# Performance work log

Measured on AMD Instinct MI355X. Metric: run time of the kernel, lower is better.

Reference implementation:

```python
import jax, jax.numpy as jnp
import numpy as np

B, C, H, W = 8, 128, 64, 64
C8, C2 = C // 8, C // 2


def conv1x1(x, w, b):
    # x: [B,Cin,H,W], w: [Cout,Cin], b: [Cout]
    return jnp.einsum('bchw,oc->bohw', x, w) + b[None, :, None, None]


def maxpool2(x):
    # 2x2 stride-2 max pool on [B,C,H,W]
    b, c, h, w = x.shape
    return x.reshape(b, c, h // 2, 2, w // 2, 2).max(axis=(3, 5))


def setup_inputs() -> dict:
    key = jax.random.key(0)
    ks = jax.random.split(key, 10)
    s_in = 1.0 / np.sqrt(C)
    s_c2 = 1.0 / np.sqrt(C2)
    return {
        'x': jax.random.normal(ks[0], (B, C, H, W), dtype=jnp.float32),
        'w_theta': jax.random.uniform(ks[1], (C8, C), jnp.float32, -s_in, s_in),
        'b_theta': jax.random.uniform(ks[2], (C8,), jnp.float32, -s_in, s_in),
        'w_phi': jax.random.uniform(ks[3], (C8, C), jnp.float32, -s_in, s_in),
        'b_phi': jax.random.uniform(ks[4], (C8,), jnp.float32, -s_in, s_in),
        'w_g': jax.random.uniform(ks[5], (C2, C), jnp.float32, -s_in, s_in),
        'b_g': jax.random.uniform(ks[6], (C2,), jnp.float32, -s_in, s_in),
        'w_attn': jax.random.uniform(ks[7], (C, C2), jnp.float32, -s_c2, s_c2),
        'b_attn': jax.random.uniform(ks[8], (C,), jnp.float32, -s_c2, s_c2),
        'sigma': jnp.zeros((1,), dtype=jnp.float32),
    }


def reference(x, w_theta, b_theta, w_phi, b_phi, w_g, b_g, w_attn, b_attn, sigma):
    b, ch, h, w = x.shape
    n, m = h * w, (h * w) // 4
    theta = conv1x1(x, w_theta, b_theta).reshape(b, ch // 8, n)          # [B,C8,N]
    phi = maxpool2(conv1x1(x, w_phi, b_phi)).reshape(b, ch // 8, m)      # [B,C8,M]
    attn = jax.nn.softmax(jnp.einsum('bdn,bdm->bnm', theta, phi), axis=-1)  # [B,N,M]
    g = maxpool2(conv1x1(x, w_g, b_g)).reshape(b, ch // 2, m)            # [B,C2,M]
    attn_g = jnp.einsum('bcm,bnm->bcn', g, attn).reshape(b, ch // 2, h, w)
    attn_g = conv1x1(attn_g, w_attn, b_attn)
    return x + sigma[0] * attn_g
```

## Files before the change

kernel.cpp:

```cpp
#include <hip/hip_runtime.h>
#include <hip/hip_bf16.h>
#include <math.h>
#include <string.h>

#define Bn 8
#define Cn 128
#define Nn 4096
#define Mn 1024
#define C8n 16
#define C2n 64

typedef __attribute__((ext_vector_type(8))) short short8;
typedef __attribute__((ext_vector_type(4))) float floatx4;
typedef __attribute__((ext_vector_type(4))) unsigned short ushortx4;

typedef const __attribute__((address_space(1))) void gv_t;
typedef __attribute__((address_space(3))) void lv_t;

__device__ __forceinline__ unsigned short f2bf(float f) {
    union { float f; unsigned u; } v; v.f = f;
    unsigned r = v.u + 0x7fff + ((v.u >> 16) & 1);
    return (unsigned short)(r >> 16);
}
__device__ __forceinline__ unsigned pk2(float a, float b) {
    __hip_bfloat162 h = __float22bfloat162_rn(make_float2(a, b));
    union { __hip_bfloat162 h2; unsigned u; } cv;
    cv.h2 = h;
    return cv.u;
}

__global__ __launch_bounds__(256) void k1_pre(
    const float* __restrict__ x,
    const float* __restrict__ w_theta, const float* __restrict__ b_theta,
    const float* __restrict__ w_phi,   const float* __restrict__ b_phi,
    const float* __restrict__ w_g,     const float* __restrict__ b_g,
    unsigned short* __restrict__ thA,
    unsigned short* __restrict__ phB,
    unsigned short* __restrict__ gB)
{
    __shared__ unsigned short wA[6 * 4 * 64 * 8];
    __shared__ unsigned short xB[8 * 4 * 64 * 8];
    __shared__ unsigned short pool[80][33];
    __shared__ float biases[96];

    const int t    = threadIdx.x;
    const int b    = blockIdx.x & 7;
    const int h2   = blockIdx.x >> 3;
    const int wv   = t >> 6;
    const int lane = t & 63;
    const int q    = lane >> 4;
    const int l15  = lane & 15;
    const float L2E = 1.4426950408889634f;

    if (t < 96)
        biases[t] = (t < 16) ? b_theta[t] * L2E
                  : (t < 32) ? b_phi[t - 16] : b_g[t - 32];

    #pragma unroll
    for (int k = 0; k < 12; ++k) {
        int u  = t + k * 256;
        int oc = u >> 5, c4 = u & 31;
        const float* src = (oc < 16) ? (w_theta + oc * Cn)
                         : (oc < 32) ? (w_phi + (oc - 16) * Cn)
                                     : (w_g + (oc - 32) * Cn);
        float4 wv4 = *(const float4*)(src + c4 * 4);
        float sc = (oc < 16) ? L2E : 1.f;
        int c = c4 * 4;
        int ot = oc >> 4, kc = c >> 5, qq = (c >> 3) & 3, jj = c & 7;
        uint2 pk = { pk2(wv4.x * sc, wv4.y * sc), pk2(wv4.z * sc, wv4.w * sc) };
        *(uint2*)(wA + (((ot * 4 + kc) * 64 + qq * 16 + (oc & 15)) * 8 + jj)) = pk;
    }

    const float* xb = x + (size_t)b * Cn * Nn + h2 * 128;
    #pragma unroll
    for (int k = 0; k < 16; ++k) {
        int u   = t + k * 256;
        int pos = u & 127, c4 = u >> 7;
        int c   = c4 * 4;
        float v0 = xb[(size_t)(c + 0) * Nn + pos];
        float v1 = xb[(size_t)(c + 1) * Nn + pos];
        float v2 = xb[(size_t)(c + 2) * Nn + pos];
        float v3 = xb[(size_t)(c + 3) * Nn + pos];
        int pt = pos >> 4, kc = c >> 5, qq = (c >> 3) & 3, jj = c & 7;
        uint2 pk = { pk2(v0, v1), pk2(v2, v3) };
        *(uint2*)(xB + (((pt * 4 + kc) * 64 + qq * 16 + (pos & 15)) * 8 + jj)) = pk;
    }
    __syncthreads();

    floatx4 acc[6][2];
    #pragma unroll
    for (int ot = 0; ot < 6; ++ot)
        #pragma unroll
        for (int p2 = 0; p2 < 2; ++p2) acc[ot][p2] = (floatx4){0.f, 0.f, 0.f, 0.f};

    #pragma unroll
    for (int kc = 0; kc < 4; ++kc) {
        short8 Bf0 = *(const short8*)(xB + ((wv * 4 + kc) * 64 + lane) * 8);
        short8 Bf1 = *(const short8*)(xB + (((wv + 4) * 4 + kc) * 64 + lane) * 8);
        #pragma unroll
        for (int ot = 0; ot < 6; ++ot) {
            short8 Af = *(const short8*)(wA + ((ot * 4 + kc) * 64 + lane) * 8);
            acc[ot][0] = __builtin_amdgcn_mfma_f32_16x16x32_bf16(Af, Bf0, acc[ot][0], 0, 0, 0);
            acc[ot][1] = __builtin_amdgcn_mfma_f32_16x16x32_bf16(Af, Bf1, acc[ot][1], 0, 0, 0);
        }
    }

    #pragma unroll
    for (int p2 = 0; p2 < 2; ++p2) {
        const int pt = wv + p2 * 4;
        float v0 = acc[0][p2][0] + biases[q * 4 + 0];
        float v1 = acc[0][p2][1] + biases[q * 4 + 1];
        float v2 = acc[0][p2][2] + biases[q * 4 + 2];
        float v3 = acc[0][p2][3] + biases[q * 4 + 3];
        uint2 pk = { pk2(v0, v1), pk2(v2, v3) };
        *(uint2*)(thA + ((((size_t)b * 256 + h2 * 8 + pt) * 2 + (q >> 1)) * 128
                         + l15 * 8 + (q & 1) * 4)) = pk;
    }

    #pragma unroll
    for (int ot = 1; ot < 6; ++ot) {
        #pragma unroll
        for (int r = 0; r < 4; ++r) {
            float vmax = fmaxf(acc[ot][0][r], acc[ot][1][r]);
            float pmax = fmaxf(vmax, __shfl_xor(vmax, 1, 64));
            if ((l15 & 1) == 0) {
                int oc = (ot - 1) * 16 + q * 4 + r;
                int w2 = wv * 8 + (l15 >> 1);
                pool[oc][w2] = f2bf(pmax + biases[16 + oc]);
            }
        }
    }
    __syncthreads();

    if (t < 64) {
        int w2h = t >> 5, ml = (t >> 1) & 15, dh = t & 1;
        int w2 = w2h * 16 + ml;
        ushortx4 lo, hi;
        #pragma unroll
        for (int j = 0; j < 4; ++j) { lo[j] = pool[dh * 8 + j][w2];
                                      hi[j] = pool[dh * 8 + 4 + j][w2]; }
        unsigned short* dst = phB + (((size_t)b * 64 + h2 * 2 + w2h) * 2 + dh) * 128 + ml * 8;
        *(ushortx4*)dst = lo;
        *(ushortx4*)(dst + 4) = hi;
    }
    {
        int c = t >> 2, sq = t & 3;
        ushortx4 lo, hi;
        #pragma unroll
        for (int j = 0; j < 8; ++j) {
            int w2 = (j & 1) * 16 + sq * 4 + (j >> 1);
            unsigned short v = pool[16 + c][w2];
            if (j < 4) lo[j] = v; else hi[j - 4] = v;
        }
        unsigned short* dst = gB + ((((size_t)b * 32 + h2) * 4 + (c >> 4)) * 4 + sq) * 128
                              + (c & 15) * 8;
        *(ushortx4*)dst = lo;
        *(ushortx4*)(dst + 4) = hi;
    }
}

__global__ __launch_bounds__(256, 4) void k2_attn(
    const float* __restrict__ x,
    const unsigned short* __restrict__ thA,
    const unsigned short* __restrict__ phB,
    const unsigned short* __restrict__ gB,
    const float* __restrict__ w_attn, const float* __restrict__ b_attn,
    const float* __restrict__ sigma_p,
    float* __restrict__ out)
{
    __shared__ __attribute__((aligned(16))) char smem[26112];
    char*  Pall  = smem + 20480;
    float* battn = (float*)(smem + 25600);

    const int tid  = threadIdx.x;
    const int wave = tid >> 6;
    const int lane = tid & 63;
    const int q    = lane >> 4;
    const int l15  = lane & 15;
    const int b    = blockIdx.x & 7;
    const int nb   = blockIdx.x >> 3;
    const int t    = wave & 1;
    const int h    = wave >> 1;
    const int ntile = nb * 2 + t;
    const int nw   = ntile * 16;
    char* Pbase = Pall + wave * 1280;

    const float sg = sigma_p[0];

    short8 thf = {};
    if (q < 2)
        thf = *(const short8*)(thA + ((((size_t)b * 256 + ntile) * 2 + q) * 16 + l15) * 8);

    floatx4 O[4];
    #pragma unroll
    for (int cs = 0; cs < 4; ++cs) O[cs] = (floatx4){0.f, 0.f, 0.f, 0.f};
    float L[4] = {0.f, 0.f, 0.f, 0.f};

    const char* phb = (const char*)(phB + (size_t)b * 16384);
    const char* gbb = (const char*)(gB  + (size_t)b * 65536);
    const char* sph = phb + h * 16384;
    const char* sgb = gbb + h * 65536;
    char* mybuf = smem + h * 10240;

    {
        const char* srcp = sph;
        const char* srcg = sgb;
        char* dst = mybuf;
        for (int j = t; j < 5; j += 2) {
            const char* src = (j == 0) ? srcp : (srcg + (j - 1) * 1024);
            __builtin_amdgcn_global_load_lds((gv_t*)(src + lane * 16),
                                             (lv_t*)(dst + j * 1024), 16, 0, 0);
        }
    }

    for (int s = 0; s < 16; ++s) {
        __syncthreads();
        if (s < 15) {
            char* dst = mybuf + ((s + 1) & 1) * 5120;
            const char* srcp = sph + (s + 1) * 1024;
            const char* srcg = sgb + (size_t)(s + 1) * 4096;
            for (int j = t; j < 5; j += 2) {
                const char* src = (j == 0) ? srcp : (srcg + (j - 1) * 1024);
                __builtin_amdgcn_global_load_lds((gv_t*)(src + lane * 16),
                                                 (lv_t*)(dst + j * 1024), 16, 0, 0);
            }
        }
        const char* cbuf = mybuf + (s & 1) * 5120;
        const unsigned short* phis = (const unsigned short*)cbuf;
        const unsigned short* gs   = (const unsigned short*)(cbuf + 1024);

        short8 bf0 = {}, bf1 = {};
        if (q < 2) {
            bf0 = *(const short8*)(phis + ((0 * 2 + q) * 16 + l15) * 8);
            bf1 = *(const short8*)(phis + ((1 * 2 + q) * 16 + l15) * 8);
        }
        floatx4 S0 = __builtin_amdgcn_mfma_f32_16x16x32_bf16(
                         thf, bf0, (floatx4){0.f, 0.f, 0.f, 0.f}, 0, 0, 0);
        floatx4 S1 = __builtin_amdgcn_mfma_f32_16x16x32_bf16(
                         thf, bf1, (floatx4){0.f, 0.f, 0.f, 0.f}, 0, 0, 0);
        #pragma unroll
        for (int r = 0; r < 4; ++r) {
            float pa = exp2f(S0[r]);
            float pb = exp2f(S1[r]);
            L[r] += pa + pb;
            *(unsigned*)(Pbase + (q * 4 + r) * 80 + l15 * 4) = pk2(pa, pb);
        }

        short8 Af = *(const short8*)(Pbase + l15 * 80 + q * 16);
        #pragma unroll
        for (int cs = 0; cs < 4; ++cs) {
            short8 Bf = *(const short8*)(gs + ((cs * 4 + q) * 16 + l15) * 8);
            O[cs] = __builtin_amdgcn_mfma_f32_16x16x32_bf16(Af, Bf, O[cs], 0, 0, 0);
        }
    }

    #pragma unroll
    for (int d = 1; d <= 8; d <<= 1)
        #pragma unroll
        for (int r = 0; r < 4; ++r) L[r] += __shfl_xor(L[r], d, 64);

    __syncthreads();
    float* Lpart = (float*)(smem + 8704);
    if (h == 1) {
        #pragma unroll
        for (int r = 0; r < 4; ++r) {
            float* Orow = (float*)(smem + t * 4352 + (q * 4 + r) * 272);
            #pragma unroll
            for (int cs = 0; cs < 4; ++cs) Orow[cs * 16 + l15] = O[cs][r];
            if (l15 == 0) Lpart[t * 16 + q * 4 + r] = L[r];
        }
    }
    if (tid < 128) battn[tid] = b_attn[tid];
    __syncthreads();
    unsigned short* Obuf = (unsigned short*)(smem + 20480);
    if (h == 0) {
        #pragma unroll
        for (int r = 0; r < 4; ++r) {
            const float* Orow = (const float*)(smem + t * 4352 + (q * 4 + r) * 272);
            #pragma unroll
            for (int cs = 0; cs < 4; ++cs) O[cs][r] += Orow[cs * 16 + l15];
            L[r] += Lpart[t * 16 + q * 4 + r];
        }
        float inv[4];
        #pragma unroll
        for (int r = 0; r < 4; ++r) inv[r] = 1.0f / L[r];
        unsigned short* Ob = Obuf + t * 1152;
        #pragma unroll
        for (int cs = 0; cs < 4; ++cs)
            #pragma unroll
            for (int r = 0; r < 4; ++r)
                Ob[(q * 4 + r) * 72 + cs * 16 + l15] = f2bf(O[cs][r] * inv[r]);
    }
    __syncthreads();

    {
        unsigned short* wAe = (unsigned short*)smem;
        #pragma unroll
        for (int k = 0; k < 8; ++k) {
            int i = tid + k * 256;
            float4 wv = ((const float4*)w_attn)[i];
            int o = i >> 4, c = (i & 15) * 4;
            uint2 pk = { pk2(wv.x, wv.y), pk2(wv.z, wv.w) };
            *(uint2*)(wAe + ((o >> 4) * 2 + (c >> 5)) * 512 + (o & 15) * 32 + (c & 31)) = pk;
        }
    }
    __syncthreads();

    {
        const unsigned short* wAe = (const unsigned short*)smem;
        const unsigned short* Ob  = Obuf + t * 1152;
        short8 B0 = *(const short8*)(Ob + l15 * 72 + q * 8);
        short8 B1 = *(const short8*)(Ob + l15 * 72 + 32 + q * 8);
        const float* xw = x   + (size_t)b * Cn * Nn + nw + l15;
        float*       ow = out + (size_t)b * Cn * Nn + nw + l15;
        #pragma unroll
        for (int ot4 = 0; ot4 < 4; ++ot4) {
            const int ot = h * 4 + ot4;
            short8 A0 = *(const short8*)(wAe + (ot * 2 + 0) * 512 + l15 * 32 + q * 8);
            short8 A1 = *(const short8*)(wAe + (ot * 2 + 1) * 512 + l15 * 32 + q * 8);
            floatx4 D = __builtin_amdgcn_mfma_f32_16x16x32_bf16(
                            A0, B0, (floatx4){0.f, 0.f, 0.f, 0.f}, 0, 0, 0);
            D = __builtin_amdgcn_mfma_f32_16x16x32_bf16(A1, B1, D, 0, 0, 0);
            #pragma unroll
            for (int r = 0; r < 4; ++r) {
                int o = ot * 16 + q * 4 + r;
                float v = D[r] + battn[o];
                ow[(size_t)o * Nn] = xw[(size_t)o * Nn] + sg * v;
            }
        }
    }
}

extern "C" void kernel_launch(void* const* d_in, const int* in_sizes, int n_in,
                              void* d_out, int out_size, void* d_ws, size_t ws_size,
                              hipStream_t stream) {
    const float* x       = (const float*)d_in[0];
    const float* w_theta = (const float*)d_in[1];
    const float* b_theta = (const float*)d_in[2];
    const float* w_phi   = (const float*)d_in[3];
    const float* b_phi   = (const float*)d_in[4];
    const float* w_g     = (const float*)d_in[5];
    const float* b_g     = (const float*)d_in[6];
    const float* w_attn  = (const float*)d_in[7];
    const float* b_attn  = (const float*)d_in[8];
    const float* sigma   = (const float*)d_in[9];
    float* out = (float*)d_out;

    unsigned short* thA = (unsigned short*)d_ws;
    unsigned short* phB = thA + 524288;
    unsigned short* gBp = phB + 131072;

    k1_pre<<<256, 256, 0, stream>>>(x, w_theta, b_theta, w_phi, b_phi,
                                    w_g, b_g, thA, phB, gBp);
    k2_attn<<<1024, 256, 0, stream>>>(x, thA, phB, gBp, w_attn, b_attn, sigma, out);
}
```

Before: 115.7 us.

## Load phi and g fragments directly from global instead of LDS staging

Removes the double-buffered global_load_lds staging of phi and g tiles, along with the per-iteration __syncthreads, and has each wave read its MFMA B fragments straight from global memory (L2/L1 cached). The loop is unrolled by two so independent loads can be issued early, and shared memory shrinks by about 4 KB, which may raise occupancy. The trade-off is that loads are duplicated across the two waves sharing the same h, and global latency is no longer hidden by explicit prefetch.

```diff
diff --git a/kernel.cpp b/kernel.cpp
--- a/kernel.cpp
+++ b/kernel.cpp
@@ -13,9 +13,6 @@
 typedef __attribute__((ext_vector_type(8))) short short8;
 typedef __attribute__((ext_vector_type(4))) float floatx4;
 typedef __attribute__((ext_vector_type(4))) unsigned short ushortx4;
-
-typedef const __attribute__((address_space(1))) void gv_t;
-typedef __attribute__((address_space(3))) void lv_t;
 
 __device__ __forceinline__ unsigned short f2bf(float f) {
     union { float f; unsigned u; } v; v.f = f;
@@ -168,9 +165,9 @@
     const float* __restrict__ sigma_p,
     float* __restrict__ out)
 {
-    __shared__ __attribute__((aligned(16))) char smem[26112];
-    char*  Pall  = smem + 20480;
-    float* battn = (float*)(smem + 25600);
+    __shared__ __attribute__((aligned(16))) char smem[22016];
+    char*  Pall  = smem + 16384;
+    float* battn = (float*)(smem + 21504);
 
     const int tid  = threadIdx.x;
     const int wave = tid >> 6;
@@ -196,44 +193,23 @@
     for (int cs = 0; cs < 4; ++cs) O[cs] = (floatx4){0.f, 0.f, 0.f, 0.f};
     float L[4] = {0.f, 0.f, 0.f, 0.f};
 
-    const char* phb = (const char*)(phB + (size_t)b * 16384);
-    const char* gbb = (const char*)(gB  + (size_t)b * 65536);
-    const char* sph = phb + h * 16384;
-    const char* sgb = gbb + h * 65536;
-    char* mybuf = smem + h * 10240;
-
-    {
-        const char* srcp = sph;
-        const char* srcg = sgb;
-        char* dst = mybuf;
-        for (int j = t; j < 5; j += 2) {
-            const char* src = (j == 0) ? srcp : (srcg + (j - 1) * 1024);
-            __builtin_amdgcn_global_load_lds((gv_t*)(src + lane * 16),
-                                             (lv_t*)(dst + j * 1024), 16, 0, 0);
-        }
-    }
-
+    const unsigned short* phh = phB + (size_t)b * 16384 + h * 32 * 256;
+    const unsigned short* ghh = gB  + (size_t)b * 65536 + h * 16 * 2048;
+
+    #pragma unroll 2
     for (int s = 0; s < 16; ++s) {
-        __syncthreads();
-        if (s < 15) {
-            char* dst = mybuf + ((s + 1) & 1) * 5120;
-            const char* srcp = sph + (s + 1) * 1024;
-            const char* srcg = sgb + (size_t)(s + 1) * 4096;
-            for (int j = t; j < 5; j += 2) {
-                const char* src = (j == 0) ? srcp : (srcg + (j - 1) * 1024);
-                __builtin_amdgcn_global_load_lds((gv_t*)(src + lane * 16),
-                                                 (lv_t*)(dst + j * 1024), 16, 0, 0);
-            }
-        }
-        const char* cbuf = mybuf + (s & 1) * 5120;
-        const unsigned short* phis = (const unsigned short*)cbuf;
-        const unsigned short* gs   = (const unsigned short*)(cbuf + 1024);
-
+        const unsigned short* pt0 = phh + s * 512;
         short8 bf0 = {}, bf1 = {};
         if (q < 2) {
-            bf0 = *(const short8*)(phis + ((0 * 2 + q) * 16 + l15) * 8);
-            bf1 = *(const short8*)(phis + ((1 * 2 + q) * 16 + l15) * 8);
-        }
+            bf0 = *(const short8*)(pt0 + (q * 16 + l15) * 8);
+            bf1 = *(const short8*)(pt0 + 256 + (q * 16 + l15) * 8);
+        }
+        const unsigned short* gc = ghh + s * 2048;
+        short8 Bf0 = *(const short8*)(gc + ((0 * 4 + q) * 16 + l15) * 8);
+        short8 Bf1 = *(const short8*)(gc + ((1 * 4 + q) * 16 + l15) * 8);
+        short8 Bf2 = *(const short8*)(gc + ((2 * 4 + q) * 16 + l15) * 8);
+        short8 Bf3 = *(const short8*)(gc + ((3 * 4 + q) * 16 + l15) * 8);
+
         floatx4 S0 = __builtin_amdgcn_mfma_f32_16x16x32_bf16(
                          thf, bf0, (floatx4){0.f, 0.f, 0.f, 0.f}, 0, 0, 0);
         floatx4 S1 = __builtin_amdgcn_mfma_f32_16x16x32_bf16(
@@ -247,11 +223,10 @@
         }
 
         short8 Af = *(const short8*)(Pbase + l15 * 80 + q * 16);
-        #pragma unroll
-        for (int cs = 0; cs < 4; ++cs) {
-            short8 Bf = *(const short8*)(gs + ((cs * 4 + q) * 16 + l15) * 8);
-            O[cs] = __builtin_amdgcn_mfma_f32_16x16x32_bf16(Af, Bf, O[cs], 0, 0, 0);
-        }
+        O[0] = __builtin_amdgcn_mfma_f32_16x16x32_bf16(Af, Bf0, O[0], 0, 0, 0);
+        O[1] = __builtin_amdgcn_mfma_f32_16x16x32_bf16(Af, Bf1, O[1], 0, 0, 0);
+        O[2] = __builtin_amdgcn_mfma_f32_16x16x32_bf16(Af, Bf2, O[2], 0, 0, 0);
+        O[3] = __builtin_amdgcn_mfma_f32_16x16x32_bf16(Af, Bf3, O[3], 0, 0, 0);
     }
 
     #pragma unroll
@@ -272,7 +247,7 @@
     }
     if (tid < 128) battn[tid] = b_attn[tid];
     __syncthreads();
-    unsigned short* Obuf = (unsigned short*)(smem + 20480);
+    unsigned short* Obuf = (unsigned short*)(smem + 16384);
     if (h == 0) {
         #pragma unroll
         for (int r = 0; r < 4; ++r) {
```

Result: faster. 110.3 us (-4.7%).
